# Optimization experiments

Hardware: AMD Instinct MI355X
Metric: run time of the kernel (lower is better)

Reference implementation:

```python
import jax, jax.numpy as jnp
import numpy as np

N_NODES = 50000
N_EDGES = 800000
NFEAT, NHID, NOUT = 128, 128, 64


def _glorot(key, shape):
    lim = 1.0 / np.sqrt(shape[0])
    return jax.random.uniform(key, shape, jnp.float32, -lim, lim)


def setup_inputs() -> dict:
    key = jax.random.key(0)
    ks = jax.random.split(key, 12)
    x = jax.random.normal(ks[0], (N_NODES, NFEAT), jnp.float32)
    edge_src = jax.random.randint(ks[1], (N_EDGES,), 0, N_NODES, jnp.int32)
    edge_dst = jax.random.randint(ks[2], (N_EDGES,), 0, N_NODES, jnp.int32)
    edge_w = jax.random.uniform(ks[3], (N_EDGES,), jnp.float32)  # normalized adj values
    # layer params: nfeat->nhid, nhid->nhid, nhid->nhid, nhid->nout
    W0, b0 = _glorot(ks[4], (NFEAT, NHID)), jnp.zeros((NHID,), jnp.float32)
    W1, b1 = _glorot(ks[5], (NHID, NHID)), jnp.zeros((NHID,), jnp.float32)
    W2, b2 = _glorot(ks[6], (NHID, NHID)), jnp.zeros((NHID,), jnp.float32)
    W3, b3 = _glorot(ks[7], (NHID, NOUT)), jnp.zeros((NOUT,), jnp.float32)
    return dict(x=x, edge_src=edge_src, edge_dst=edge_dst, edge_w=edge_w,
                W0=W0, b0=b0, W1=W1, b1=b1, W2=W2, b2=b2, W3=W3, b3=b3)


def _gcn_layer(h, src, dst, w, W, b):
    # support = h @ W ; out = A @ support + b  (A given as weighted edge list)
    support = h @ W                               # [N, d_out]
    msgs = support[src] * w[:, None]              # [E, d_out] gather + scale
    agg = jax.ops.segment_sum(msgs, dst, num_segments=N_NODES)  # scatter-add
    return agg + b


def reference(x, edge_src, edge_dst, edge_w, W0, b0, W1, b1, W2, b2, W3, b3):
    # eval mode: dropout is identity
    h = jax.nn.relu(_gcn_layer(x, edge_src, edge_dst, edge_w, W0, b0))
    h = jax.nn.relu(_gcn_layer(h, edge_src, edge_dst, edge_w, W1, b1))
    h = jax.nn.relu(_gcn_layer(h, edge_src, edge_dst, edge_w, W2, b2))
    h = _gcn_layer(h, edge_src, edge_dst, edge_w, W3, b3)  # no relu on last layer
    return h
```

## Files before the change

### kernel.cpp

```cpp
#include <hip/hip_runtime.h>


constexpr int NN = 50000;
constexpr int NE = 800000;
constexpr int NB = (NN + 127) >> 7;
constexpr int CAP = 4608;
constexpr int PART_CHUNK = 4096;
constexpr int PART_GRID = (NE + PART_CHUNK - 1) / PART_CHUNK;

typedef __attribute__((ext_vector_type(8))) short bf16x8;
typedef __attribute__((ext_vector_type(4))) float floatx4;

__device__ inline unsigned short f2bf(float f) {
    unsigned u = __float_as_uint(f);
    u += 0x7fffu + ((u >> 16) & 1u);
    return (unsigned short)(u >> 16);
}
__device__ inline float bflo(unsigned v) { return __uint_as_float(v << 16); }
__device__ inline float bfhi(unsigned v) { return __uint_as_float(v & 0xffff0000u); }


__global__ __launch_bounds__(256) void k_part(
        const int* __restrict__ src, const int* __restrict__ dst,
        const float* __restrict__ w, int* __restrict__ bfill,
        int2* __restrict__ ep) {
    __shared__ int hist[NB], base[NB], off[NB];
    int tid = threadIdx.x;
    for (int b = tid; b < NB; b += 256) { hist[b] = 0; off[b] = 0; }
    __syncthreads();

    int e0 = blockIdx.x * PART_CHUNK;
    int  sreg[16]; int wreg[16]; short breg[16];
#pragma unroll
    for (int i = 0; i < 16; ++i) {
        int e = e0 + i * 256 + tid;
        if (e < NE) {
            int d = dst[e];
            int b = d >> 7;
            sreg[i] = (src[e] & 0xffff) | ((d & 127) << 16);
            wreg[i] = __float_as_int(w[e]);
            breg[i] = (short)b;
            atomicAdd(&hist[b], 1);
        } else breg[i] = -1;
    }
    __syncthreads();
    for (int b = tid; b < NB; b += 256)
        base[b] = b * CAP + atomicAdd(&bfill[b], hist[b]);
    __syncthreads();
#pragma unroll
    for (int i = 0; i < 16; ++i) {
        if (breg[i] >= 0) {
            int b = breg[i];
            int p = atomicAdd(&off[b], 1);
            ep[base[b] + p] = make_int2(sreg[i], wreg[i]);
        }
    }
}

__global__ __launch_bounds__(256) void k_sort(
        const int2* __restrict__ ep, const int* __restrict__ bfill,
        unsigned* __restrict__ es, int2* __restrict__ begend) {
    __shared__ int cnt[128], base[128], fl[128];
    __shared__ int s_total;
    int b  = blockIdx.x;
    int n0 = b << 7;
    int nn = min(128, NN - n0);
    int t  = threadIdx.x;
    if (t < 128) { cnt[t] = 0; fl[t] = 0; }
    __syncthreads();
    int bbase = b * CAP;
    int beg = bbase, end = bbase + bfill[b];
    for (int e = beg + t; e < end; e += 256)
        atomicAdd(&cnt[(ep[e].x >> 16) & 127], 1);
    __syncthreads();
    int cp = (t < 128) ? ((cnt[t] + 15) & ~15) : 0;
    if (t < 128) base[t] = cp;
    __syncthreads();
    for (int off = 1; off < 128; off <<= 1) {
        int add = (t >= off && t < 128) ? base[t - off] : 0;
        __syncthreads();
        if (t < 128) base[t] += add;
        __syncthreads();
    }
    if (t == 127) s_total = base[127];
    __syncthreads();
    int total = s_total;
    for (int i = t; i < total + 16; i += 256) es[bbase + i] = 0u;
    if (t < nn) {
        int off = base[t] - cp;
        begend[n0 + t] = make_int2(bbase + off, bbase + off + cp);
    }
    __syncthreads();
    for (int e = beg + t; e < end; e += 256) {
        int2 v = ep[e];
        int d = (v.x >> 16) & 127;
        int off = base[d] - ((cnt[d] + 15) & ~15);
        int pos = bbase + off + atomicAdd(&fl[d], 1);
        es[pos] = (unsigned)(v.x & 0xffff) |
                  ((unsigned)f2bf(__int_as_float(v.y)) << 16);
    }
}


__global__ void k_prep(
        const float* __restrict__ W0, const float* __restrict__ W1,
        const float* __restrict__ W2, const float* __restrict__ W3,
        unsigned short* __restrict__ T0, unsigned short* __restrict__ T1,
        unsigned short* __restrict__ T2, unsigned short* __restrict__ T3,
        int* __restrict__ bfill) {
    int b = blockIdx.x;
    if (b == 448) {
        for (int i = threadIdx.x; i < NB; i += 128) bfill[i] = 0;
        return;
    }
    const float* W; unsigned short* T; int N, n;
    if (b < 128)      { W = W0; T = T0; N = 128; n = b; }
    else if (b < 256) { W = W1; T = T1; N = 128; n = b - 128; }
    else if (b < 384) { W = W2; T = T2; N = 128; n = b - 256; }
    else              { W = W3; T = T3; N = 64;  n = b - 384; }
    int k = threadIdx.x;
    T[n * 128 + k] = f2bf(W[(size_t)k * N + n]);
}


__device__ inline bf16x8 ldA_f32(const float* A, size_t off) {
    float4 u = *(const float4*)&A[off];
    float4 v = *(const float4*)&A[off + 4];
    bf16x8 r;
    r[0] = (short)f2bf(u.x); r[1] = (short)f2bf(u.y);
    r[2] = (short)f2bf(u.z); r[3] = (short)f2bf(u.w);
    r[4] = (short)f2bf(v.x); r[5] = (short)f2bf(v.y);
    r[6] = (short)f2bf(v.z); r[7] = (short)f2bf(v.w);
    return r;
}

__global__ __launch_bounds__(256) void k_gemm0(
        const float* __restrict__ A,
        const unsigned short* __restrict__ Wt,
        unsigned short* __restrict__ C,
        int M) {
    constexpr int STR = 136;
    __shared__ unsigned short sWt[128 * STR];

    const int tid = threadIdx.x;
#pragma unroll
    for (int i = 0; i < 8; ++i) {
        int c = i * 256 + tid;
        int row = c >> 4, col = (c & 15) * 8;
        *(uint4*)&sWt[row * STR + col] = *(const uint4*)&Wt[row * 128 + col];
    }

    const int wv = tid >> 6;
    const int ln = tid & 63;
    const int m  = ln & 15;
    const int qd = ln >> 4;

    int gr  = blockIdx.x * 64 + wv * 16 + m;
    int grc = (gr < M) ? gr : (M - 1);
    bf16x8 af[4];
#pragma unroll
    for (int s = 0; s < 4; ++s)
        af[s] = ldA_f32(A, (size_t)grc * 128 + s * 32 + qd * 8);

    __syncthreads();

    floatx4 acc[8];
#pragma unroll
    for (int c = 0; c < 8; ++c) {
        acc[c] = (floatx4){0.f, 0.f, 0.f, 0.f};
#pragma unroll
        for (int s = 0; s < 4; ++s) {
            bf16x8 bf = *(const bf16x8*)&sWt[(c * 16 + m) * STR + s * 32 + qd * 8];
            acc[c] = __builtin_amdgcn_mfma_f32_16x16x32_bf16(af[s], bf, acc[c], 0, 0, 0);
        }
    }

    int row0 = blockIdx.x * 64 + wv * 16 + qd * 4;
#pragma unroll
    for (int c = 0; c < 8; ++c)
#pragma unroll
        for (int r = 0; r < 4; ++r) {
            int row = row0 + r;
            if (row < M) C[(size_t)row * 128 + c * 16 + m] = f2bf(acc[c][r]);
        }
}


#define FMA8(W, R)                                                              \
    acc[0] = fmaf(W, bflo((R).x), acc[0]); acc[1] = fmaf(W, bfhi((R).x), acc[1]); \
    acc[2] = fmaf(W, bflo((R).y), acc[2]); acc[3] = fmaf(W, bfhi((R).y), acc[3]); \
    acc[4] = fmaf(W, bflo((R).z), acc[4]); acc[5] = fmaf(W, bfhi((R).z), acc[5]); \
    acc[6] = fmaf(W, bflo((R).w), acc[6]); acc[7] = fmaf(W, bfhi((R).w), acc[7]);

template<int NOUT>
__global__ __launch_bounds__(128, 4) void k_fused(
        const unsigned short* __restrict__ sup,
        const int2* __restrict__ begend, const unsigned* __restrict__ es,
        const float* __restrict__ bias,
        const unsigned short* __restrict__ Wt,
        unsigned short* __restrict__ C,
        int M) {
    constexpr int NT  = NOUT / 16;
    constexpr int STR = 136;
    __shared__ unsigned short hT[16 * STR];

    const int tid = threadIdx.x;
    const int wv  = tid >> 6;
    const int ln  = tid & 63;
    const int g   = ln >> 4;
    const int l   = ln & 15;

    const int n0 = blockIdx.x * 16;
    int2 be = begend[n0 + wv * 8];

    for (int nn = 0; nn < 8; ++nn) {
        int n = n0 + wv * 8 + nn;
        int beg = be.x, endp = be.y;
        if (nn < 7) be = begend[n + 1];
        float acc[8] = {0.f, 0.f, 0.f, 0.f, 0.f, 0.f, 0.f, 0.f};
        if (endp > beg) {
            int e = beg;
            uint4 mv = *(const uint4*)&es[e + 4 * g];
            for (;;) {
                uint4 r0 = *(const uint4*)&sup[(size_t)(mv.x & 0xffffu) * 128 + l * 8];
                uint4 r1 = *(const uint4*)&sup[(size_t)(mv.y & 0xffffu) * 128 + l * 8];
                uint4 r2 = *(const uint4*)&sup[(size_t)(mv.z & 0xffffu) * 128 + l * 8];
                uint4 r3 = *(const uint4*)&sup[(size_t)(mv.w & 0xffffu) * 128 + l * 8];
                float w0 = bfhi(mv.x), w1 = bfhi(mv.y);
                float w2 = bfhi(mv.z), w3 = bfhi(mv.w);
                e += 16;
                bool more = e < endp;
                uint4 mn = *(const uint4*)&es[e + 4 * g];
                FMA8(w0, r0); FMA8(w1, r1); FMA8(w2, r2); FMA8(w3, r3);
                mv = mn;
                if (!more) break;
            }
#pragma unroll
            for (int f = 0; f < 8; ++f) {
                acc[f] += __shfl_xor(acc[f], 16, 64);
                acc[f] += __shfl_xor(acc[f], 32, 64);
            }
        }
        if (g == 0) {
            unsigned pk[4];
#pragma unroll
            for (int q = 0; q < 4; ++q) {
                float a0 = fmaxf(acc[2 * q]     + bias[l * 8 + 2 * q],     0.f);
                float a1 = fmaxf(acc[2 * q + 1] + bias[l * 8 + 2 * q + 1], 0.f);
                pk[q] = (unsigned)f2bf(a0) | ((unsigned)f2bf(a1) << 16);
            }
            *(uint4*)&hT[(wv * 8 + nn) * STR + l * 8] = *(uint4*)pk;
        }
    }
    __syncthreads();

    const int m_ = ln & 15, qd = ln >> 4;
    const int c0 = wv * (NT / 2);
    bf16x8 af[4];
#pragma unroll
    for (int s = 0; s < 4; ++s)
        af[s] = *(const bf16x8*)&hT[m_ * STR + s * 32 + qd * 8];

    floatx4 acc2[NT / 2];
#pragma unroll
    for (int c = 0; c < NT / 2; ++c) {
        acc2[c] = (floatx4){0.f, 0.f, 0.f, 0.f};
#pragma unroll
        for (int s = 0; s < 4; ++s) {
            bf16x8 bf = *(const bf16x8*)&Wt[(size_t)((c0 + c) * 16 + m_) * 128 + s * 32 + qd * 8];
            acc2[c] = __builtin_amdgcn_mfma_f32_16x16x32_bf16(af[s], bf, acc2[c], 0, 0, 0);
        }
    }
    int row0 = n0 + qd * 4;
#pragma unroll
    for (int c = 0; c < NT / 2; ++c)
#pragma unroll
        for (int r = 0; r < 4; ++r) {
            int row = row0 + r;
            if (row < M) C[(size_t)row * NOUT + (c0 + c) * 16 + m_] = f2bf(acc2[c][r]);
        }
}


__global__ __launch_bounds__(256, 4) void k_agg64(
        const unsigned short* __restrict__ sup,
        const int2* __restrict__ begend, const unsigned* __restrict__ es,
        const float* __restrict__ bias, float* __restrict__ out) {
    int n  = blockIdx.x * 4 + (threadIdx.x >> 6);
    int ln = threadIdx.x & 63;
    int g  = ln >> 3, l = ln & 7;
    int2 be = begend[n];
    int beg = be.x, endp = be.y;
    float acc[8] = {0.f, 0.f, 0.f, 0.f, 0.f, 0.f, 0.f, 0.f};
    if (endp > beg) {
        int e = beg;
        uint2 mv = *(const uint2*)&es[e + 2 * g];
        for (;;) {
            uint4 r0 = *(const uint4*)&sup[(size_t)(mv.x & 0xffffu) * 64 + l * 8];
            uint4 r1 = *(const uint4*)&sup[(size_t)(mv.y & 0xffffu) * 64 + l * 8];
            float w0 = bfhi(mv.x), w1 = bfhi(mv.y);
            e += 16;
            bool more = e < endp;
            uint2 mn = *(const uint2*)&es[e + 2 * g];
            FMA8(w0, r0); FMA8(w1, r1);
            mv = mn;
            if (!more) break;
        }
    }
#pragma unroll
    for (int f = 0; f < 8; ++f) {
        acc[f] += __shfl_xor(acc[f], 8, 64);
        acc[f] += __shfl_xor(acc[f], 16, 64);
        acc[f] += __shfl_xor(acc[f], 32, 64);
    }
    if (g == 0) {
        float4 o0 = make_float4(acc[0] + bias[l * 8],     acc[1] + bias[l * 8 + 1],
                                acc[2] + bias[l * 8 + 2], acc[3] + bias[l * 8 + 3]);
        float4 o1 = make_float4(acc[4] + bias[l * 8 + 4], acc[5] + bias[l * 8 + 5],
                                acc[6] + bias[l * 8 + 6], acc[7] + bias[l * 8 + 7]);
        *(float4*)&out[(size_t)n * 64 + l * 8]     = o0;
        *(float4*)&out[(size_t)n * 64 + l * 8 + 4] = o1;
    }
}


extern "C" void kernel_launch(void* const* d_in, const int* in_sizes, int n_in,
                              void* d_out, int out_size, void* d_ws, size_t ws_size,
                              hipStream_t stream) {
    (void)in_sizes; (void)n_in; (void)out_size; (void)ws_size;

    const float* x    = (const float*)d_in[0];
    const int*   esrc = (const int*)d_in[1];
    const int*   edst = (const int*)d_in[2];
    const float* ew   = (const float*)d_in[3];
    const float* W0   = (const float*)d_in[4];
    const float* b0   = (const float*)d_in[5];
    const float* W1   = (const float*)d_in[6];
    const float* b1   = (const float*)d_in[7];
    const float* W2   = (const float*)d_in[8];
    const float* b2   = (const float*)d_in[9];
    const float* W3   = (const float*)d_in[10];
    const float* b3   = (const float*)d_in[11];

    char* p = (char*)d_ws;
    auto alloc = [&](size_t bytes) {
        char* r = p;
        p += (bytes + 511) & ~size_t(511);
        return r;
    };
    int*      bfill  = (int*)     alloc((size_t)NB * 4);
    int2*     begend = (int2*)    alloc((size_t)NN * 8);
    int2*     ep     = (int2*)    alloc((size_t)NB * CAP * 8);
    unsigned* es     = (unsigned*)alloc((size_t)NB * CAP * 4);
    unsigned short* sA  = (unsigned short*)alloc((size_t)NN * 128 * 2);
    unsigned short* sB  = (unsigned short*)alloc((size_t)NN * 128 * 2);
    unsigned short* Wt0 = (unsigned short*)alloc((size_t)128 * 128 * 2);
    unsigned short* Wt1 = (unsigned short*)alloc((size_t)128 * 128 * 2);
    unsigned short* Wt2 = (unsigned short*)alloc((size_t)128 * 128 * 2);
    unsigned short* Wt3 = (unsigned short*)alloc((size_t)64 * 128 * 2);

    k_prep<<<449, 128, 0, stream>>>(W0, W1, W2, W3, Wt0, Wt1, Wt2, Wt3, bfill);
    k_part<<<PART_GRID, 256, 0, stream>>>(esrc, edst, ew, bfill, ep);
    k_sort<<<NB, 256, 0, stream>>>(ep, bfill, es, begend);

    const int g0_grid = (NN + 63) / 64;
    const int f_grid  = (NN + 15) / 16;
    const int a_grid  = (NN + 3) / 4;

    k_gemm0<<<g0_grid, 256, 0, stream>>>(x, Wt0, sA, NN);
    k_fused<128><<<f_grid, 128, 0, stream>>>(sA, begend, es, b0, Wt1, sB, NN);
    k_fused<128><<<f_grid, 128, 0, stream>>>(sB, begend, es, b1, Wt2, sA, NN);
    k_fused<64><<<f_grid, 128, 0, stream>>>(sA, begend, es, b2, Wt3, sB, NN);
    k_agg64<<<a_grid, 256, 0, stream>>>(sB, begend, es, b3, (float*)d_out);
}
```

Measured before the change: 254.8 us.

## Unfuse aggregation from GEMM and split aggregation across column groups

Replaces the fused aggregate-then-GEMM kernels with separate aggregation and GEMM kernels. Each aggregation block now handles only a 32-column slice, so every gather is a 4-byte load per lane instead of 16 bytes. This yields four times more blocks, gives each thread two accumulators instead of eight, and raises the occupancy target. The cost is that each edge-list entry is re-read once per column group, gathers are narrower and less efficient per transaction, and intermediate features take an extra global round trip through the new GEMM launches.

```diff
diff --git a/kernel.cpp b/kernel.cpp
--- a/kernel.cpp
+++ b/kernel.cpp
@@ -186,23 +186,69 @@
 }
 
 
-#define FMA8(W, R)                                                              \
-    acc[0] = fmaf(W, bflo((R).x), acc[0]); acc[1] = fmaf(W, bfhi((R).x), acc[1]); \
-    acc[2] = fmaf(W, bflo((R).y), acc[2]); acc[3] = fmaf(W, bfhi((R).y), acc[3]); \
-    acc[4] = fmaf(W, bflo((R).z), acc[4]); acc[5] = fmaf(W, bfhi((R).z), acc[5]); \
-    acc[6] = fmaf(W, bflo((R).w), acc[6]); acc[7] = fmaf(W, bfhi((R).w), acc[7]);
-
 template<int NOUT>
-__global__ __launch_bounds__(128, 4) void k_fused(
-        const unsigned short* __restrict__ sup,
-        const int2* __restrict__ begend, const unsigned* __restrict__ es,
-        const float* __restrict__ bias,
+__global__ __launch_bounds__(256) void k_gemmB(
+        const unsigned short* __restrict__ A,
         const unsigned short* __restrict__ Wt,
         unsigned short* __restrict__ C,
         int M) {
     constexpr int NT  = NOUT / 16;
     constexpr int STR = 136;
-    __shared__ unsigned short hT[16 * STR];
+    __shared__ unsigned short sWt[NOUT * STR];
+
+    const int tid = threadIdx.x;
+#pragma unroll
+    for (int i = 0; i < NOUT * 16 / 256; ++i) {
+        int c = i * 256 + tid;
+        int row = c >> 4, col = (c & 15) * 8;
+        *(uint4*)&sWt[row * STR + col] = *(const uint4*)&Wt[row * 128 + col];
+    }
+
+    const int wv = tid >> 6;
+    const int ln = tid & 63;
+    const int m  = ln & 15;
+    const int qd = ln >> 4;
+
+    int gr  = blockIdx.x * 64 + wv * 16 + m;
+    int grc = (gr < M) ? gr : (M - 1);
+    bf16x8 af[4];
+#pragma unroll
+    for (int s = 0; s < 4; ++s)
+        af[s] = *(const bf16x8*)&A[(size_t)grc * 128 + s * 32 + qd * 8];
+
+    __syncthreads();
+
+    floatx4 acc[NT];
+#pragma unroll
+    for (int c = 0; c < NT; ++c) {
+        acc[c] = (floatx4){0.f, 0.f, 0.f, 0.f};
+#pragma unroll
+        for (int s = 0; s < 4; ++s) {
+            bf16x8 bf = *(const bf16x8*)&sWt[(c * 16 + m) * STR + s * 32 + qd * 8];
+            acc[c] = __builtin_amdgcn_mfma_f32_16x16x32_bf16(af[s], bf, acc[c], 0, 0, 0);
+        }
+    }
+
+    int row0 = blockIdx.x * 64 + wv * 16 + qd * 4;
+#pragma unroll
+    for (int c = 0; c < NT; ++c)
+#pragma unroll
+        for (int r = 0; r < 4; ++r) {
+            int row = row0 + r;
+            if (row < M) C[(size_t)row * NOUT + c * 16 + m] = f2bf(acc[c][r]);
+        }
+}
+
+
+__global__ __launch_bounds__(128, 8) void k_aggc(
+        const unsigned short* __restrict__ sup,
+        const int2* __restrict__ begend, const unsigned* __restrict__ es,
+        const float* __restrict__ bias,
+        unsigned short* __restrict__ out,
+        int M) {
+    const int grp  = blockIdx.x & 3;
+    const int tile = blockIdx.x >> 2;
+    const int col0 = grp * 32;
 
     const int tid = threadIdx.x;
     const int wv  = tid >> 6;
@@ -210,116 +256,96 @@
     const int g   = ln >> 4;
     const int l   = ln & 15;
 
-    const int n0 = blockIdx.x * 16;
+    const int n0 = tile * 16;
     int2 be = begend[n0 + wv * 8];
 
     for (int nn = 0; nn < 8; ++nn) {
         int n = n0 + wv * 8 + nn;
         int beg = be.x, endp = be.y;
         if (nn < 7) be = begend[n + 1];
-        float acc[8] = {0.f, 0.f, 0.f, 0.f, 0.f, 0.f, 0.f, 0.f};
+        float a0 = 0.f, a1 = 0.f;
         if (endp > beg) {
             int e = beg;
             uint4 mv = *(const uint4*)&es[e + 4 * g];
             for (;;) {
-                uint4 r0 = *(const uint4*)&sup[(size_t)(mv.x & 0xffffu) * 128 + l * 8];
-                uint4 r1 = *(const uint4*)&sup[(size_t)(mv.y & 0xffffu) * 128 + l * 8];
-                uint4 r2 = *(const uint4*)&sup[(size_t)(mv.z & 0xffffu) * 128 + l * 8];
-                uint4 r3 = *(const uint4*)&sup[(size_t)(mv.w & 0xffffu) * 128 + l * 8];
+                unsigned r0 = *(const unsigned*)&sup[(size_t)(mv.x & 0xffffu) * 128 + col0 + l * 2];
+                unsigned r1 = *(const unsigned*)&sup[(size_t)(mv.y & 0xffffu) * 128 + col0 + l * 2];
+                unsigned r2 = *(const unsigned*)&sup[(size_t)(mv.z & 0xffffu) * 128 + col0 + l * 2];
+                unsigned r3 = *(const unsigned*)&sup[(size_t)(mv.w & 0xffffu) * 128 + col0 + l * 2];
                 float w0 = bfhi(mv.x), w1 = bfhi(mv.y);
                 float w2 = bfhi(mv.z), w3 = bfhi(mv.w);
                 e += 16;
                 bool more = e < endp;
                 uint4 mn = *(const uint4*)&es[e + 4 * g];
-                FMA8(w0, r0); FMA8(w1, r1); FMA8(w2, r2); FMA8(w3, r3);
+                a0 = fmaf(w0, bflo(r0), a0); a1 = fmaf(w0, bfhi(r0), a1);
+                a0 = fmaf(w1, bflo(r1), a0); a1 = fmaf(w1, bfhi(r1), a1);
+                a0 = fmaf(w2, bflo(r2), a0); a1 = fmaf(w2, bfhi(r2), a1);
+                a0 = fmaf(w3, bflo(r3), a0); a1 = fmaf(w3, bfhi(r3), a1);
                 mv = mn;
                 if (!more) break;
             }
-#pragma unroll
-            for (int f = 0; f < 8; ++f) {
-                acc[f] += __shfl_xor(acc[f], 16, 64);
-                acc[f] += __shfl_xor(acc[f], 32, 64);
-            }
-        }
-        if (g == 0) {
-            unsigned pk[4];
-#pragma unroll
-            for (int q = 0; q < 4; ++q) {
-                float a0 = fmaxf(acc[2 * q]     + bias[l * 8 + 2 * q],     0.f);
-                float a1 = fmaxf(acc[2 * q + 1] + bias[l * 8 + 2 * q + 1], 0.f);
-                pk[q] = (unsigned)f2bf(a0) | ((unsigned)f2bf(a1) << 16);
-            }
-            *(uint4*)&hT[(wv * 8 + nn) * STR + l * 8] = *(uint4*)pk;
-        }
-    }
-    __syncthreads();
-
-    const int m_ = ln & 15, qd = ln >> 4;
-    const int c0 = wv * (NT / 2);
-    bf16x8 af[4];
-#pragma unroll
-    for (int s = 0; s < 4; ++s)
-        af[s] = *(const bf16x8*)&hT[m_ * STR + s * 32 + qd * 8];
-
-    floatx4 acc2[NT / 2];
-#pragma unroll
-    for (int c = 0; c < NT / 2; ++c) {
-        acc2[c] = (floatx4){0.f, 0.f, 0.f, 0.f};
-#pragma unroll
-        for (int s = 0; s < 4; ++s) {
-            bf16x8 bf = *(const bf16x8*)&Wt[(size_t)((c0 + c) * 16 + m_) * 128 + s * 32 + qd * 8];
-            acc2[c] = __builtin_amdgcn_mfma_f32_16x16x32_bf16(af[s], bf, acc2[c], 0, 0, 0);
-        }
-    }
-    int row0 = n0 + qd * 4;
-#pragma unroll
-    for (int c = 0; c < NT / 2; ++c)
-#pragma unroll
-        for (int r = 0; r < 4; ++r) {
-            int row = row0 + r;
-            if (row < M) C[(size_t)row * NOUT + (c0 + c) * 16 + m_] = f2bf(acc2[c][r]);
-        }
-}
-
-
-__global__ __launch_bounds__(256, 4) void k_agg64(
+            a0 += __shfl_xor(a0, 16, 64); a1 += __shfl_xor(a1, 16, 64);
+            a0 += __shfl_xor(a0, 32, 64); a1 += __shfl_xor(a1, 32, 64);
+        }
+        if (g == 0 && n < M) {
+            a0 = fmaxf(a0 + bias[col0 + l * 2],     0.f);
+            a1 = fmaxf(a1 + bias[col0 + l * 2 + 1], 0.f);
+            unsigned pk = (unsigned)f2bf(a0) | ((unsigned)f2bf(a1) << 16);
+            *(unsigned*)&out[(size_t)n * 128 + col0 + l * 2] = pk;
+        }
+    }
+}
+
+__global__ __launch_bounds__(128, 8) void k_agg64c(
         const unsigned short* __restrict__ sup,
         const int2* __restrict__ begend, const unsigned* __restrict__ es,
         const float* __restrict__ bias, float* __restrict__ out) {
-    int n  = blockIdx.x * 4 + (threadIdx.x >> 6);
-    int ln = threadIdx.x & 63;
-    int g  = ln >> 3, l = ln & 7;
-    int2 be = begend[n];
-    int beg = be.x, endp = be.y;
-    float acc[8] = {0.f, 0.f, 0.f, 0.f, 0.f, 0.f, 0.f, 0.f};
-    if (endp > beg) {
-        int e = beg;
-        uint2 mv = *(const uint2*)&es[e + 2 * g];
-        for (;;) {
-            uint4 r0 = *(const uint4*)&sup[(size_t)(mv.x & 0xffffu) * 64 + l * 8];
-            uint4 r1 = *(const uint4*)&sup[(size_t)(mv.y & 0xffffu) * 64 + l * 8];
-            float w0 = bfhi(mv.x), w1 = bfhi(mv.y);
-            e += 16;
-            bool more = e < endp;
-            uint2 mn = *(const uint2*)&es[e + 2 * g];
-            FMA8(w0, r0); FMA8(w1, r1);
-            mv = mn;
-            if (!more) break;
-        }
-    }
-#pragma unroll
-    for (int f = 0; f < 8; ++f) {
-        acc[f] += __shfl_xor(acc[f], 8, 64);
-        acc[f] += __shfl_xor(acc[f], 16, 64);
-        acc[f] += __shfl_xor(acc[f], 32, 64);
-    }
-    if (g == 0) {
-        float4 o0 = make_float4(acc[0] + bias[l * 8],     acc[1] + bias[l * 8 + 1],
-                                acc[2] + bias[l * 8 + 2], acc[3] + bias[l * 8 + 3]);
-        float4 o1 = make_float4(acc[4] + bias[l * 8 + 4], acc[5] + bias[l * 8 + 5],
-                                acc[6] + bias[l * 8 + 6], acc[7] + bias[l * 8 + 7]);
-        *(float4*)&out[(size_t)n * 64 + l * 8]     = o0;
-        *(float4*)&out[(size_t)n * 64 + l * 8 + 4] = o1;
+    const int grp  = blockIdx.x & 1;
+    const int tile = blockIdx.x >> 1;
+    const int col0 = grp * 32;
+
+    const int tid = threadIdx.x;
+    const int wv  = tid >> 6;
+    const int ln  = tid & 63;
+    const int g   = ln >> 4;
+    const int l   = ln & 15;
+
+    const int n0 = tile * 16;
+    int2 be = begend[n0 + wv * 8];
+
+    for (int nn = 0; nn < 8; ++nn) {
+        int n = n0 + wv * 8 + nn;
+        int beg = be.x, endp = be.y;
+        if (nn < 7) be = begend[n + 1];
+        float a0 = 0.f, a1 = 0.f;
+        if (endp > beg) {
+            int e = beg;
+            uint4 mv = *(const uint4*)&es[e + 4 * g];
+            for (;;) {
+                unsigned r0 = *(const unsigned*)&sup[(size_t)(mv.x & 0xffffu) * 64 + col0 + l * 2];
+                unsigned r1 = *(const unsigned*)&sup[(size_t)(mv.y & 0xffffu) * 64 + col0 + l * 2];
+                unsigned r2 = *(const unsigned*)&sup[(size_t)(mv.z & 0xffffu) * 64 + col0 + l * 2];
+                unsigned r3 = *(const unsigned*)&sup[(size_t)(mv.w & 0xffffu) * 64 + col0 + l * 2];
+                float w0 = bfhi(mv.x), w1 = bfhi(mv.y);
+                float w2 = bfhi(mv.z), w3 = bfhi(mv.w);
+                e += 16;
+                bool more = e < endp;
+                uint4 mn = *(const uint4*)&es[e + 4 * g];
+                a0 = fmaf(w0, bflo(r0), a0); a1 = fmaf(w0, bfhi(r0), a1);
+                a0 = fmaf(w1, bflo(r1), a0); a1 = fmaf(w1, bfhi(r1), a1);
+                a0 = fmaf(w2, bflo(r2), a0); a1 = fmaf(w2, bfhi(r2), a1);
+                a0 = fmaf(w3, bflo(r3), a0); a1 = fmaf(w3, bfhi(r3), a1);
+                mv = mn;
+                if (!more) break;
+            }
+            a0 += __shfl_xor(a0, 16, 64); a1 += __shfl_xor(a1, 16, 64);
+            a0 += __shfl_xor(a0, 32, 64); a1 += __shfl_xor(a1, 32, 64);
+        }
+        if (g == 0 && n < NN) {
+            float2 o = make_float2(a0 + bias[col0 + l * 2],
+                                   a1 + bias[col0 + l * 2 + 1]);
+            *(float2*)&out[(size_t)n * 64 + col0 + l * 2] = o;
+        }
     }
 }
 
@@ -352,8 +378,8 @@
     int2*     begend = (int2*)    alloc((size_t)NN * 8);
     int2*     ep     = (int2*)    alloc((size_t)NB * CAP * 8);
     unsigned* es     = (unsigned*)alloc((size_t)NB * CAP * 4);
-    unsigned short* sA  = (unsigned short*)alloc((size_t)NN * 128 * 2);
-    unsigned short* sB  = (unsigned short*)alloc((size_t)NN * 128 * 2);
+    unsigned short* sup = (unsigned short*)alloc((size_t)NN * 128 * 2);
+    unsigned short* hb  = (unsigned short*)alloc((size_t)NN * 128 * 2);
     unsigned short* Wt0 = (unsigned short*)alloc((size_t)128 * 128 * 2);
     unsigned short* Wt1 = (unsigned short*)alloc((size_t)128 * 128 * 2);
     unsigned short* Wt2 = (unsigned short*)alloc((size_t)128 * 128 * 2);
@@ -363,13 +389,16 @@
     k_part<<<PART_GRID, 256, 0, stream>>>(esrc, edst, ew, bfill, ep);
     k_sort<<<NB, 256, 0, stream>>>(ep, bfill, es, begend);
 
-    const int g0_grid = (NN + 63) / 64;
-    const int f_grid  = (NN + 15) / 16;
-    const int a_grid  = (NN + 3) / 4;
-
-    k_gemm0<<<g0_grid, 256, 0, stream>>>(x, Wt0, sA, NN);
-    k_fused<128><<<f_grid, 128, 0, stream>>>(sA, begend, es, b0, Wt1, sB, NN);
-    k_fused<128><<<f_grid, 128, 0, stream>>>(sB, begend, es, b1, Wt2, sA, NN);
-    k_fused<64><<<f_grid, 128, 0, stream>>>(sA, begend, es, b2, Wt3, sB, NN);
-    k_agg64<<<a_grid, 256, 0, stream>>>(sB, begend, es, b3, (float*)d_out);
-}
+    const int gemm_grid = (NN + 63) / 64;
+    const int aggc_grid = ((NN + 15) / 16) * 4;
+    const int a64_grid  = ((NN + 15) / 16) * 2;
+
+    k_gemm0<<<gemm_grid, 256, 0, stream>>>(x, Wt0, sup, NN);
+    k_aggc<<<aggc_grid, 128, 0, stream>>>(sup, begend, es, b0, hb, NN);
+    k_gemmB<128><<<gemm_grid, 256, 0, stream>>>(hb, Wt1, sup, NN);
+    k_aggc<<<aggc_grid, 128, 0, stream>>>(sup, begend, es, b1, hb, NN);
+    k_gemmB<128><<<gemm_grid, 256, 0, stream>>>(hb, Wt2, sup, NN);
+    k_aggc<<<aggc_grid, 128, 0, stream>>>(sup, begend, es, b2, hb, NN);
+    k_gemmB<64><<<gemm_grid, 256, 0, stream>>>(hb, Wt3, sup, NN);
+    k_agg64c<<<a64_grid, 128, 0, stream>>>(sup, begend, es, b3, (float*)d_out);
+}
```

After: 368.6 us. +44.6%, slower.
